# Kernel tuning notes

Hardware: AMD Instinct MI355X
Metric: run time of the kernel (lower is better)

The kernel has to match this reference:

```python
import jax, jax.numpy as jnp
import numpy as np

N_DOMAINS = 8
LN_EPS = 1e-5


def setup_inputs() -> dict:
    key = jax.random.key(0)
    ks = jax.random.split(key, 4)
    N, D_IN, D_HID, D_OUT = 32768, 256, 1024, 256
    x = jax.random.normal(ks[0], (N, D_IN), dtype=jnp.float32)
    domain_types = jax.random.randint(ks[1], (N,), 0, N_DOMAINS, dtype=jnp.int32)
    # Per-domain MLP parameters (8 independent experts)
    W1 = jax.random.normal(ks[2], (N_DOMAINS, D_IN, D_HID), dtype=jnp.float32) * (1.0 / np.sqrt(D_IN))
    b1 = jnp.zeros((N_DOMAINS, D_HID), dtype=jnp.float32)
    gamma = jnp.ones((N_DOMAINS, D_HID), dtype=jnp.float32)
    beta = jnp.zeros((N_DOMAINS, D_HID), dtype=jnp.float32)
    W2 = jax.random.normal(ks[3], (N_DOMAINS, D_HID, D_OUT), dtype=jnp.float32) * (1.0 / np.sqrt(D_HID))
    b2 = jnp.zeros((N_DOMAINS, D_OUT), dtype=jnp.float32)
    return {"x": x, "domain_types": domain_types, "W1": W1, "b1": b1,
            "gamma": gamma, "beta": beta, "W2": W2, "b2": b2}


def _expert_mlp(x, W1d, b1d, gd, bd, W2d, b2d):
    # Linear -> LayerNorm -> ReLU -> (Dropout: identity at eval) -> Linear
    h = x @ W1d + b1d                       # [N, hid]
    mu = jnp.mean(h, axis=-1, keepdims=True)
    var = jnp.mean(jnp.square(h - mu), axis=-1, keepdims=True)
    h = (h - mu) * jax.lax.rsqrt(var + LN_EPS) * gd + bd
    h = jax.nn.relu(h)
    return h @ W2d + b2d                    # [N, out]


def reference(x, domain_types, W1, b1, gamma, beta, W2, b2):
    # output dim == x.shape[-1] (as in the torch code: zeros(batch, x.shape[-1]))
    out = jnp.zeros((x.shape[0], x.shape[-1]), dtype=x.dtype)
    for d in range(N_DOMAINS):  # small fixed expert loop (static MoE dispatch)
        y = _expert_mlp(x, W1[d], b1[d], gamma[d], beta[d], W2[d], b2[d])
        mask = (domain_types == d)[:, None]
        out = jnp.where(mask, y, out)
    return out
```

## Files before the change

### kernel.cpp

```cpp
#include <hip/hip_runtime.h>
#include <hip/hip_bf16.h>


#define ND 8
#define NROWS 32768
#define DIN 256
#define DHID 1024
#define DOUT 256
#define MPAD 33792
#define NTILES 264

typedef short short8 __attribute__((ext_vector_type(8)));
typedef unsigned short ushort8v __attribute__((ext_vector_type(8)));
typedef float floatx4 __attribute__((ext_vector_type(4)));

__device__ __forceinline__ unsigned short f2bf(float f) {
    unsigned u = __builtin_bit_cast(unsigned, f);
    unsigned r = u + 0x7fff + ((u >> 16) & 1);
    return (unsigned short)(r >> 16);
}
__device__ __forceinline__ float bf2f(unsigned short h) {
    unsigned u = ((unsigned)h) << 16;
    return __builtin_bit_cast(float, u);
}

#define GLDS16(gp, lp) __builtin_amdgcn_global_load_lds( \
    (const __attribute__((address_space(1))) void*)(gp), \
    (__attribute__((address_space(3))) void*)(lp), 16, 0, 0)

__global__ void transpose_both(const float* __restrict__ W1,
                               const float* __restrict__ W2,
                               unsigned short* __restrict__ W1T,
                               unsigned short* __restrict__ W2T,
                               int* __restrict__ cnt) {
    __shared__ float t[32][33];
    const int z = blockIdx.z;
    const bool isW1 = z < ND;
    const int d = isW1 ? z : z - ND;
    const int R = isW1 ? DIN : DHID;
    const int C = isW1 ? DHID : DOUT;
    const int r0 = (isW1 ? blockIdx.x : blockIdx.y) * 32;
    const int c0 = (isW1 ? blockIdx.y : blockIdx.x) * 32;
    const int tx = threadIdx.x & 31, ty = threadIdx.x >> 5;
    if (z == 0 && blockIdx.x == 0 && blockIdx.y == 0 && threadIdx.x < 16)
        cnt[threadIdx.x] = 0;
    const float* src = (isW1 ? W1 : W2) + (size_t)d * R * C;
    unsigned short* dst = (isW1 ? W1T : W2T) + (size_t)d * R * C;
#pragma unroll
    for (int i = 0; i < 32; i += 8)
        t[ty + i][tx] = src[(size_t)(r0 + ty + i) * C + c0 + tx];
    __syncthreads();
#pragma unroll
    for (int i = 0; i < 32; i += 8)
        dst[(size_t)(c0 + ty + i) * R + r0 + tx] = f2bf(t[tx][ty + i]);
}

__global__ void histo(const int* __restrict__ dt, int* __restrict__ counts) {
    __shared__ int lc[ND];
    if (threadIdx.x < ND) lc[threadIdx.x] = 0;
    __syncthreads();
    int i = blockIdx.x * 256 + threadIdx.x;
    atomicAdd(&lc[dt[i]], 1);
    __syncthreads();
    if (threadIdx.x < ND) atomicAdd(&counts[threadIdx.x], lc[threadIdx.x]);
}

__global__ void make_meta(const int* __restrict__ counts, int* __restrict__ cursors,
                          int2* __restrict__ meta, int* __restrict__ perm) {
    __shared__ int ps[ND], pe[ND];
    if (threadIdx.x == 0) {
        int off = 0, t = 0;
        for (int d = 0; d < ND; d++) {
            cursors[d] = off;
            int nt = (counts[d] + 127) >> 7;
            for (int i = 0; i < nt; i++) meta[t++] = make_int2(d, off + (i << 7));
            ps[d] = off + counts[d];
            pe[d] = off + (nt << 7);
            off += nt << 7;
        }
        for (; t < NTILES; t++) meta[t] = make_int2(-1, 0);
    }
    __syncthreads();
#pragma unroll
    for (int d = 0; d < ND; d++)
        for (int p = ps[d] + threadIdx.x; p < pe[d]; p += 256) perm[p] = -1;
}

__global__ __launch_bounds__(256)
void assign_pos(const int* __restrict__ dt, int* __restrict__ cursors,
                int* __restrict__ perm, int* __restrict__ pos) {
    __shared__ int lcnt[ND];
    __shared__ int lbase[ND];
    const int tid = threadIdx.x;
    if (tid < ND) lcnt[tid] = 0;
    __syncthreads();
    const int r = blockIdx.x * 256 + tid;
    const int d = dt[r];
    const int myrank = atomicAdd(&lcnt[d], 1);
    __syncthreads();
    if (tid < ND && lcnt[tid] > 0)
        lbase[tid] = atomicAdd(&cursors[tid], lcnt[tid]);
    __syncthreads();
    const int p = lbase[d] + myrank;
    pos[r] = p;
    perm[p] = r;
}

__global__ __launch_bounds__(256)
void copy_rows(const float* __restrict__ x, const int* __restrict__ pos,
               unsigned short* __restrict__ xs) {
    const int tid = threadIdx.x;
    const int lane = tid & 63;
    const int r = blockIdx.x * 4 + (tid >> 6);
    const int p = pos[r];
    float4 v = ((const float4*)(x + (size_t)r * DIN))[lane];
    ushort4 o;
    o.x = f2bf(v.x); o.y = f2bf(v.y); o.z = f2bf(v.z); o.w = f2bf(v.w);
    ((ushort4*)(xs + (size_t)p * DIN))[lane] = o;
}

__global__ __launch_bounds__(256, 2)
void gemm_a(const unsigned short* __restrict__ A,
            const unsigned short* __restrict__ Bt,
            const float* __restrict__ bias,
            const int2* __restrict__ meta,
            unsigned short* __restrict__ H,
            float2* __restrict__ stats) {
    const int2 md = meta[blockIdx.x];
    const int dom = md.x;
    if (dom < 0) return;
    const int m0 = md.y;
    const int n0 = blockIdx.y * 256;

    __shared__ unsigned short As[128 * 32];
    __shared__ unsigned short Bs[256 * 32];

    const int tid = threadIdx.x;
    const int lane = tid & 63;
    const int w = tid >> 6;
    const int wr = w >> 1, wc = w & 1;
    const int c16 = lane & 15, quad = lane >> 4;

    const unsigned short* Abase = A + (size_t)m0 * DIN;
    const unsigned short* Bbase = Bt + (size_t)dom * DHID * DIN + (size_t)n0 * DIN;

    floatx4 acc[4][8];
#pragma unroll
    for (int i = 0; i < 4; i++)
#pragma unroll
        for (int j = 0; j < 8; j++) acc[i][j] = 0.f;

    for (int k0 = 0; k0 < DIN; k0 += 32) {
#pragma unroll
        for (int it = 0; it < 2; ++it) {
            const int c = w * 128 + it * 64 + lane;
            const int m = c >> 2, kc = c & 3;
            GLDS16(Abase + (size_t)m * DIN + k0 + kc * 8, &As[(w * 128 + it * 64) * 8]);
        }
#pragma unroll
        for (int it = 0; it < 4; ++it) {
            const int c = w * 256 + it * 64 + lane;
            const int n = c >> 2, kc = c & 3;
            GLDS16(Bbase + (size_t)n * DIN + k0 + kc * 8, &Bs[(w * 256 + it * 64) * 8]);
        }
        __syncthreads();

        short8 a[4], b[8];
        const int kk = quad * 8;
#pragma unroll
        for (int i = 0; i < 4; i++)
            a[i] = *(const short8*)&As[(wr * 64 + i * 16 + c16) * 32 + kk];
#pragma unroll
        for (int j = 0; j < 8; j++)
            b[j] = *(const short8*)&Bs[(wc * 128 + j * 16 + c16) * 32 + kk];
#pragma unroll
        for (int i = 0; i < 4; i++)
#pragma unroll
            for (int j = 0; j < 8; j++)
                acc[i][j] = __builtin_amdgcn_mfma_f32_16x16x32_bf16(a[i], b[j], acc[i][j], 0, 0, 0);
        __syncthreads();
    }

    float bv[8];
#pragma unroll
    for (int j = 0; j < 8; j++)
        bv[j] = bias[dom * DHID + n0 + wc * 128 + j * 16 + c16];

    float2* st = stats + (size_t)(blockIdx.y * 2 + wc) * MPAD;
#pragma unroll
    for (int i = 0; i < 4; i++) {
        const int rowbase = m0 + wr * 64 + i * 16 + quad * 4;
#pragma unroll
        for (int r = 0; r < 4; r++) {
            float s = 0.f, q = 0.f;
            unsigned short* hrow = H + (size_t)(rowbase + r) * DHID + n0 + wc * 128;
#pragma unroll
            for (int j = 0; j < 8; j++) {
                const float v = acc[i][j][r] + bv[j];
                hrow[j * 16 + c16] = f2bf(v);
                s += v; q += v * v;
            }
#pragma unroll
            for (int o = 1; o < 16; o <<= 1) {
                s += __shfl_xor(s, o, 64);
                q += __shfl_xor(q, o, 64);
            }
            if (c16 == 0) st[rowbase + r] = make_float2(s, q);
        }
    }
}

__global__ __launch_bounds__(256, 1)
void gemm_b_ln(const unsigned short* __restrict__ H,
               const unsigned short* __restrict__ Bt,
               const float* __restrict__ bias,
               const float* __restrict__ gamma,
               const float* __restrict__ beta,
               const float2* __restrict__ stats,
               const int2* __restrict__ meta,
               const int* __restrict__ perm,
               float* __restrict__ out) {
    const int2 md = meta[blockIdx.x];
    const int dom = md.x;
    if (dom < 0) return;
    const int m0 = md.y;

    __shared__ unsigned short As[128 * 32];
    __shared__ unsigned short Bs[256 * 32];
    __shared__ unsigned short gsh[DHID];
    __shared__ unsigned short bsh[DHID];
    __shared__ float mu_s[128], rs_s[128];

    const int tid = threadIdx.x;
    const int lane = tid & 63;
    const int w = tid >> 6;
    const int wr = w >> 1, wc = w & 1;
    const int c16 = lane & 15, quad = lane >> 4;

    if (tid < 128) {
        float s = 0.f, q = 0.f;
#pragma unroll
        for (int cb = 0; cb < 8; cb++) {
            const float2 p = stats[(size_t)cb * MPAD + m0 + tid];
            s += p.x; q += p.y;
        }
        const float inv = 1.0f / (float)DHID;
        const float mu = s * inv;
        const float var = fmaxf(q * inv - mu * mu, 0.f);
        mu_s[tid] = mu;
        rs_s[tid] = rsqrtf(var + 1e-5f);
    }
    {
        const int base = tid * 4;
        const float4 g4 = *(const float4*)(gamma + dom * DHID + base);
        const float4 b4 = *(const float4*)(beta + dom * DHID + base);
        gsh[base + 0] = f2bf(g4.x); gsh[base + 1] = f2bf(g4.y);
        gsh[base + 2] = f2bf(g4.z); gsh[base + 3] = f2bf(g4.w);
        bsh[base + 0] = f2bf(b4.x); bsh[base + 1] = f2bf(b4.y);
        bsh[base + 2] = f2bf(b4.z); bsh[base + 3] = f2bf(b4.w);
    }
    __syncthreads();

    const unsigned short* Hbase = H + (size_t)m0 * DHID;
    const unsigned short* Bbase = Bt + (size_t)dom * DOUT * DHID;

    floatx4 acc[4][8];
#pragma unroll
    for (int i = 0; i < 4; i++)
#pragma unroll
        for (int j = 0; j < 8; j++) acc[i][j] = 0.f;

    const int c0i = tid, c1i = 256 + tid;
    const int row0 = c0i >> 2, kg0 = c0i & 3;
    const int row1 = c1i >> 2, kg1 = c1i & 3;
    ushort8v hv0 = *(const ushort8v*)(Hbase + (size_t)row0 * DHID + kg0 * 8);
    ushort8v hv1 = *(const ushort8v*)(Hbase + (size_t)row1 * DHID + kg1 * 8);

    for (int k0 = 0; k0 < DHID; k0 += 32) {
        {
            const float mu0 = mu_s[row0], rs0 = rs_s[row0];
            const float mu1 = mu_s[row1], rs1 = rs_s[row1];
            const ushort8v g0 = *(const ushort8v*)&gsh[k0 + kg0 * 8];
            const ushort8v b0 = *(const ushort8v*)&bsh[k0 + kg0 * 8];
            const ushort8v g1 = *(const ushort8v*)&gsh[k0 + kg1 * 8];
            const ushort8v b1v = *(const ushort8v*)&bsh[k0 + kg1 * 8];
            ushort8v o0, o1;
#pragma unroll
            for (int e = 0; e < 8; e++) {
                const float t0 = (bf2f(hv0[e]) - mu0) * rs0;
                o0[e] = f2bf(fmaxf(t0 * bf2f(g0[e]) + bf2f(b0[e]), 0.f));
                const float t1 = (bf2f(hv1[e]) - mu1) * rs1;
                o1[e] = f2bf(fmaxf(t1 * bf2f(g1[e]) + bf2f(b1v[e]), 0.f));
            }
            *(ushort8v*)&As[row0 * 32 + kg0 * 8] = o0;
            *(ushort8v*)&As[row1 * 32 + kg1 * 8] = o1;
        }
#pragma unroll
        for (int it = 0; it < 4; ++it) {
            const int c = w * 256 + it * 64 + lane;
            const int n = c >> 2, kc = c & 3;
            GLDS16(Bbase + (size_t)n * DHID + k0 + kc * 8, &Bs[(w * 256 + it * 64) * 8]);
        }
        if (k0 + 32 < DHID) {
            hv0 = *(const ushort8v*)(Hbase + (size_t)row0 * DHID + k0 + 32 + kg0 * 8);
            hv1 = *(const ushort8v*)(Hbase + (size_t)row1 * DHID + k0 + 32 + kg1 * 8);
        }
        __syncthreads();

        short8 a[4], b[8];
        const int kk = quad * 8;
#pragma unroll
        for (int i = 0; i < 4; i++)
            a[i] = *(const short8*)&As[(wr * 64 + i * 16 + c16) * 32 + kk];
#pragma unroll
        for (int j = 0; j < 8; j++)
            b[j] = *(const short8*)&Bs[(wc * 128 + j * 16 + c16) * 32 + kk];
#pragma unroll
        for (int i = 0; i < 4; i++)
#pragma unroll
            for (int j = 0; j < 8; j++)
                acc[i][j] = __builtin_amdgcn_mfma_f32_16x16x32_bf16(a[i], b[j], acc[i][j], 0, 0, 0);
        __syncthreads();
    }

    float bv[8];
#pragma unroll
    for (int j = 0; j < 8; j++)
        bv[j] = bias[dom * DOUT + wc * 128 + j * 16 + c16];
#pragma unroll
    for (int i = 0; i < 4; i++) {
        const int rowbase = m0 + wr * 64 + i * 16 + quad * 4;
#pragma unroll
        for (int r = 0; r < 4; r++) {
            const int orig = perm[rowbase + r];
            if (orig < 0) continue;
#pragma unroll
            for (int j = 0; j < 8; j++) {
                const int col = wc * 128 + j * 16 + c16;
                out[(size_t)orig * DOUT + col] = acc[i][j][r] + bv[j];
            }
        }
    }
}

extern "C" void kernel_launch(void* const* d_in, const int* in_sizes, int n_in,
                              void* d_out, int out_size, void* d_ws, size_t ws_size,
                              hipStream_t stream) {
    const float* x = (const float*)d_in[0];
    const int* dt = (const int*)d_in[1];
    const float* W1 = (const float*)d_in[2];
    const float* b1 = (const float*)d_in[3];
    const float* gamma = (const float*)d_in[4];
    const float* beta = (const float*)d_in[5];
    const float* W2 = (const float*)d_in[6];
    const float* b2 = (const float*)d_in[7];
    float* out = (float*)d_out;

    char* ws = (char*)d_ws;
    size_t off = 0;
    auto take = [&](size_t nbytes) -> char* {
        char* p = ws + off;
        off = (off + nbytes + 255) & ~(size_t)255;
        return p;
    };
    unsigned short* W1T = (unsigned short*)take((size_t)ND * DHID * DIN * 2);
    unsigned short* W2T = (unsigned short*)take((size_t)ND * DOUT * DHID * 2);
    unsigned short* XS  = (unsigned short*)take((size_t)MPAD * DIN * 2);
    unsigned short* H   = (unsigned short*)take((size_t)MPAD * DHID * 2);
    float2* STATS = (float2*)take((size_t)8 * MPAD * 8);
    int* PERM   = (int*)take(MPAD * 4);
    int* POS    = (int*)take(NROWS * 4);
    int* CNT    = (int*)take(64);
    int2* META  = (int2*)take(NTILES * 8);
    (void)ws_size; (void)n_in; (void)in_sizes; (void)out_size;

    int* COUNTS = CNT;
    int* CURSORS = CNT + 8;

    transpose_both<<<dim3(8, 32, 16), 256, 0, stream>>>(W1, W2, W1T, W2T, CNT);
    histo<<<NROWS / 256, 256, 0, stream>>>(dt, COUNTS);
    make_meta<<<1, 256, 0, stream>>>(COUNTS, CURSORS, META, PERM);
    assign_pos<<<NROWS / 256, 256, 0, stream>>>(dt, CURSORS, PERM, POS);
    copy_rows<<<NROWS / 4, 256, 0, stream>>>(x, POS, XS);
    gemm_a<<<dim3(NTILES, 4), 256, 0, stream>>>(XS, W1T, b1, META, H, STATS);
    gemm_b_ln<<<NTILES, 256, 0, stream>>>(
        H, W2T, b2, gamma, beta, STATS, META, PERM, out);
}
```

Measured before the change: 246.9 us.

## Split LayerNorm out of second GEMM, fuse histogram and row-copy kernels

Merges the histogram into the weight-transpose launch as an extra z-slice, and merges position assignment with the bf16 row copy so the pos buffer and one launch go away. The LayerNorm+ReLU that ran inside the second GEMM's k-loop becomes a separate in-place pass over H. The second GEMM becomes a plain 128x128 tile GEMM with async global-to-LDS loads for both operands, giving twice as many blocks and higher occupancy. In exchange, H now takes an extra read and write through global memory, and the row copy uses only 128 blocks.

```diff
diff --git a/kernel.cpp b/kernel.cpp
--- a/kernel.cpp
+++ b/kernel.cpp
@@ -28,13 +28,25 @@
     (const __attribute__((address_space(1))) void*)(gp), \
     (__attribute__((address_space(3))) void*)(lp), 16, 0, 0)
 
-__global__ void transpose_both(const float* __restrict__ W1,
-                               const float* __restrict__ W2,
-                               unsigned short* __restrict__ W1T,
-                               unsigned short* __restrict__ W2T,
-                               int* __restrict__ cnt) {
+__global__ void transpose_histo(const float* __restrict__ W1,
+                                const float* __restrict__ W2,
+                                unsigned short* __restrict__ W1T,
+                                unsigned short* __restrict__ W2T,
+                                const int* __restrict__ dt,
+                                int* __restrict__ counts) {
+    const int z = blockIdx.z;
+    if (z == 16) {
+        const int bid = blockIdx.y * 8 + blockIdx.x;
+        if (bid >= NROWS / 256) return;
+        __shared__ int lc[ND];
+        if (threadIdx.x < ND) lc[threadIdx.x] = 0;
+        __syncthreads();
+        atomicAdd(&lc[dt[bid * 256 + threadIdx.x]], 1);
+        __syncthreads();
+        if (threadIdx.x < ND) atomicAdd(&counts[threadIdx.x], lc[threadIdx.x]);
+        return;
+    }
     __shared__ float t[32][33];
-    const int z = blockIdx.z;
     const bool isW1 = z < ND;
     const int d = isW1 ? z : z - ND;
     const int R = isW1 ? DIN : DHID;
@@ -42,8 +54,6 @@
     const int r0 = (isW1 ? blockIdx.x : blockIdx.y) * 32;
     const int c0 = (isW1 ? blockIdx.y : blockIdx.x) * 32;
     const int tx = threadIdx.x & 31, ty = threadIdx.x >> 5;
-    if (z == 0 && blockIdx.x == 0 && blockIdx.y == 0 && threadIdx.x < 16)
-        cnt[threadIdx.x] = 0;
     const float* src = (isW1 ? W1 : W2) + (size_t)d * R * C;
     unsigned short* dst = (isW1 ? W1T : W2T) + (size_t)d * R * C;
 #pragma unroll
@@ -53,16 +63,6 @@
 #pragma unroll
     for (int i = 0; i < 32; i += 8)
         dst[(size_t)(c0 + ty + i) * R + r0 + tx] = f2bf(t[tx][ty + i]);
-}
-
-__global__ void histo(const int* __restrict__ dt, int* __restrict__ counts) {
-    __shared__ int lc[ND];
-    if (threadIdx.x < ND) lc[threadIdx.x] = 0;
-    __syncthreads();
-    int i = blockIdx.x * 256 + threadIdx.x;
-    atomicAdd(&lc[dt[i]], 1);
-    __syncthreads();
-    if (threadIdx.x < ND) atomicAdd(&counts[threadIdx.x], lc[threadIdx.x]);
 }
 
 __global__ void make_meta(const int* __restrict__ counts, int* __restrict__ cursors,
@@ -87,10 +87,11 @@
 }
 
 __global__ __launch_bounds__(256)
-void assign_pos(const int* __restrict__ dt, int* __restrict__ cursors,
-                int* __restrict__ perm, int* __restrict__ pos) {
-    __shared__ int lcnt[ND];
-    __shared__ int lbase[ND];
+void assign_copy(const float* __restrict__ x, const int* __restrict__ dt,
+                 int* __restrict__ cursors, int* __restrict__ perm,
+                 unsigned short* __restrict__ xs) {
+    __shared__ int lcnt[ND], lbase[ND];
+    __shared__ int spos[256];
     const int tid = threadIdx.x;
     if (tid < ND) lcnt[tid] = 0;
     __syncthreads();
@@ -102,21 +103,20 @@
         lbase[tid] = atomicAdd(&cursors[tid], lcnt[tid]);
     __syncthreads();
     const int p = lbase[d] + myrank;
-    pos[r] = p;
+    spos[tid] = p;
     perm[p] = r;
-}
-
-__global__ __launch_bounds__(256)
-void copy_rows(const float* __restrict__ x, const int* __restrict__ pos,
-               unsigned short* __restrict__ xs) {
-    const int tid = threadIdx.x;
+    __syncthreads();
     const int lane = tid & 63;
-    const int r = blockIdx.x * 4 + (tid >> 6);
-    const int p = pos[r];
-    float4 v = ((const float4*)(x + (size_t)r * DIN))[lane];
-    ushort4 o;
-    o.x = f2bf(v.x); o.y = f2bf(v.y); o.z = f2bf(v.z); o.w = f2bf(v.w);
-    ((ushort4*)(xs + (size_t)p * DIN))[lane] = o;
+    const int sub = tid >> 6;
+    for (int it = 0; it < 64; ++it) {
+        const int lr = it * 4 + sub;
+        const int gr = blockIdx.x * 256 + lr;
+        const int pp = spos[lr];
+        float4 v = ((const float4*)(x + (size_t)gr * DIN))[lane];
+        ushort4 o;
+        o.x = f2bf(v.x); o.y = f2bf(v.y); o.z = f2bf(v.z); o.w = f2bf(v.w);
+        ((ushort4*)(xs + (size_t)pp * DIN))[lane] = o;
+    }
 }
 
 __global__ __launch_bounds__(256, 2)
@@ -210,26 +210,69 @@
     }
 }
 
-__global__ __launch_bounds__(256, 1)
-void gemm_b_ln(const unsigned short* __restrict__ H,
-               const unsigned short* __restrict__ Bt,
-               const float* __restrict__ bias,
-               const float* __restrict__ gamma,
-               const float* __restrict__ beta,
-               const float2* __restrict__ stats,
-               const int2* __restrict__ meta,
-               const int* __restrict__ perm,
-               float* __restrict__ out) {
+__global__ __launch_bounds__(256)
+void ln_relu(unsigned short* __restrict__ H,
+             const float* __restrict__ gamma, const float* __restrict__ beta,
+             const float2* __restrict__ stats, const int2* __restrict__ meta) {
+    const int2 md = meta[blockIdx.x >> 2];
+    const int dom = md.x;
+    if (dom < 0) return;
+    const int m0 = md.y + (blockIdx.x & 3) * 32;
+
+    __shared__ float mu_s[32], rs_s[32];
+    const int tid = threadIdx.x;
+    if (tid < 32) {
+        float s = 0.f, q = 0.f;
+#pragma unroll
+        for (int cb = 0; cb < 8; cb++) {
+            const float2 p = stats[(size_t)cb * MPAD + m0 + tid];
+            s += p.x; q += p.y;
+        }
+        const float inv = 1.0f / (float)DHID;
+        const float mu = s * inv;
+        const float var = fmaxf(q * inv - mu * mu, 0.f);
+        mu_s[tid] = mu;
+        rs_s[tid] = rsqrtf(var + 1e-5f);
+    }
+    const int cc = (tid & 127) * 8;
+    const float4 g0 = *(const float4*)(gamma + dom * DHID + cc);
+    const float4 g1 = *(const float4*)(gamma + dom * DHID + cc + 4);
+    const float4 b0 = *(const float4*)(beta + dom * DHID + cc);
+    const float4 b1 = *(const float4*)(beta + dom * DHID + cc + 4);
+    const float gg[8] = {g0.x, g0.y, g0.z, g0.w, g1.x, g1.y, g1.z, g1.w};
+    const float bb[8] = {b0.x, b0.y, b0.z, b0.w, b1.x, b1.y, b1.z, b1.w};
+    __syncthreads();
+
+    const int half = tid >> 7;
+#pragma unroll 4
+    for (int it = 0; it < 16; ++it) {
+        const int lr = it * 2 + half;
+        unsigned short* hp = H + (size_t)(m0 + lr) * DHID + cc;
+        const ushort8v hv = *(const ushort8v*)hp;
+        const float mu = mu_s[lr], rs = rs_s[lr];
+        ushort8v o;
+#pragma unroll
+        for (int e = 0; e < 8; e++)
+            o[e] = f2bf(fmaxf((bf2f(hv[e]) - mu) * rs * gg[e] + bb[e], 0.f));
+        *(ushort8v*)hp = o;
+    }
+}
+
+__global__ __launch_bounds__(256, 2)
+void gemm_bt(const unsigned short* __restrict__ A,
+             const unsigned short* __restrict__ Bt,
+             const float* __restrict__ bias,
+             const int2* __restrict__ meta,
+             const int* __restrict__ perm,
+             float* __restrict__ out) {
     const int2 md = meta[blockIdx.x];
     const int dom = md.x;
     if (dom < 0) return;
     const int m0 = md.y;
+    const int n0 = blockIdx.y * 128;
 
     __shared__ unsigned short As[128 * 32];
-    __shared__ unsigned short Bs[256 * 32];
-    __shared__ unsigned short gsh[DHID];
-    __shared__ unsigned short bsh[DHID];
-    __shared__ float mu_s[128], rs_s[128];
+    __shared__ unsigned short Bs[128 * 32];
 
     const int tid = threadIdx.x;
     const int lane = tid & 63;
@@ -237,96 +280,40 @@
     const int wr = w >> 1, wc = w & 1;
     const int c16 = lane & 15, quad = lane >> 4;
 
-    if (tid < 128) {
-        float s = 0.f, q = 0.f;
-#pragma unroll
-        for (int cb = 0; cb < 8; cb++) {
-            const float2 p = stats[(size_t)cb * MPAD + m0 + tid];
-            s += p.x; q += p.y;
-        }
-        const float inv = 1.0f / (float)DHID;
-        const float mu = s * inv;
-        const float var = fmaxf(q * inv - mu * mu, 0.f);
-        mu_s[tid] = mu;
-        rs_s[tid] = rsqrtf(var + 1e-5f);
-    }
-    {
-        const int base = tid * 4;
-        const float4 g4 = *(const float4*)(gamma + dom * DHID + base);
-        const float4 b4 = *(const float4*)(beta + dom * DHID + base);
-        gsh[base + 0] = f2bf(g4.x); gsh[base + 1] = f2bf(g4.y);
-        gsh[base + 2] = f2bf(g4.z); gsh[base + 3] = f2bf(g4.w);
-        bsh[base + 0] = f2bf(b4.x); bsh[base + 1] = f2bf(b4.y);
-        bsh[base + 2] = f2bf(b4.z); bsh[base + 3] = f2bf(b4.w);
-    }
-    __syncthreads();
-
-    const unsigned short* Hbase = H + (size_t)m0 * DHID;
-    const unsigned short* Bbase = Bt + (size_t)dom * DOUT * DHID;
-
-    floatx4 acc[4][8];
+    const unsigned short* Abase = A + (size_t)m0 * DHID;
+    const unsigned short* Bbase = Bt + (size_t)dom * DOUT * DHID + (size_t)n0 * DHID;
+
+    floatx4 acc[4][4];
 #pragma unroll
     for (int i = 0; i < 4; i++)
 #pragma unroll
-        for (int j = 0; j < 8; j++) acc[i][j] = 0.f;
-
-    const int c0i = tid, c1i = 256 + tid;
-    const int row0 = c0i >> 2, kg0 = c0i & 3;
-    const int row1 = c1i >> 2, kg1 = c1i & 3;
-    ushort8v hv0 = *(const ushort8v*)(Hbase + (size_t)row0 * DHID + kg0 * 8);
-    ushort8v hv1 = *(const ushort8v*)(Hbase + (size_t)row1 * DHID + kg1 * 8);
+        for (int j = 0; j < 4; j++) acc[i][j] = 0.f;
 
     for (int k0 = 0; k0 < DHID; k0 += 32) {
-        {
-            const float mu0 = mu_s[row0], rs0 = rs_s[row0];
-            const float mu1 = mu_s[row1], rs1 = rs_s[row1];
-            const ushort8v g0 = *(const ushort8v*)&gsh[k0 + kg0 * 8];
-            const ushort8v b0 = *(const ushort8v*)&bsh[k0 + kg0 * 8];
-            const ushort8v g1 = *(const ushort8v*)&gsh[k0 + kg1 * 8];
-            const ushort8v b1v = *(const ushort8v*)&bsh[k0 + kg1 * 8];
-            ushort8v o0, o1;
-#pragma unroll
-            for (int e = 0; e < 8; e++) {
-                const float t0 = (bf2f(hv0[e]) - mu0) * rs0;
-                o0[e] = f2bf(fmaxf(t0 * bf2f(g0[e]) + bf2f(b0[e]), 0.f));
-                const float t1 = (bf2f(hv1[e]) - mu1) * rs1;
-                o1[e] = f2bf(fmaxf(t1 * bf2f(g1[e]) + bf2f(b1v[e]), 0.f));
-            }
-            *(ushort8v*)&As[row0 * 32 + kg0 * 8] = o0;
-            *(ushort8v*)&As[row1 * 32 + kg1 * 8] = o1;
-        }
-#pragma unroll
-        for (int it = 0; it < 4; ++it) {
-            const int c = w * 256 + it * 64 + lane;
-            const int n = c >> 2, kc = c & 3;
-            GLDS16(Bbase + (size_t)n * DHID + k0 + kc * 8, &Bs[(w * 256 + it * 64) * 8]);
-        }
-        if (k0 + 32 < DHID) {
-            hv0 = *(const ushort8v*)(Hbase + (size_t)row0 * DHID + k0 + 32 + kg0 * 8);
-            hv1 = *(const ushort8v*)(Hbase + (size_t)row1 * DHID + k0 + 32 + kg1 * 8);
-        }
-        __syncthreads();
-
-        short8 a[4], b[8];
+#pragma unroll
+        for (int it = 0; it < 2; ++it) {
+            const int c = w * 128 + it * 64 + lane;
+            const int m = c >> 2, kc = c & 3;
+            GLDS16(Abase + (size_t)m * DHID + k0 + kc * 8, &As[(w * 128 + it * 64) * 8]);
+            GLDS16(Bbase + (size_t)m * DHID + k0 + kc * 8, &Bs[(w * 128 + it * 64) * 8]);
+        }
+        __syncthreads();
+
+        short8 a[4], b[4];
         const int kk = quad * 8;
 #pragma unroll
+        for (int i = 0; i < 4; i++) {
+            a[i] = *(const short8*)&As[(wr * 64 + i * 16 + c16) * 32 + kk];
+            b[i] = *(const short8*)&Bs[(wc * 64 + i * 16 + c16) * 32 + kk];
+        }
+#pragma unroll
         for (int i = 0; i < 4; i++)
-            a[i] = *(const short8*)&As[(wr * 64 + i * 16 + c16) * 32 + kk];
-#pragma unroll
-        for (int j = 0; j < 8; j++)
-            b[j] = *(const short8*)&Bs[(wc * 128 + j * 16 + c16) * 32 + kk];
-#pragma unroll
-        for (int i = 0; i < 4; i++)
-#pragma unroll
-            for (int j = 0; j < 8; j++)
+#pragma unroll
+            for (int j = 0; j < 4; j++)
                 acc[i][j] = __builtin_amdgcn_mfma_f32_16x16x32_bf16(a[i], b[j], acc[i][j], 0, 0, 0);
         __syncthreads();
     }
 
-    float bv[8];
-#pragma unroll
-    for (int j = 0; j < 8; j++)
-        bv[j] = bias[dom * DOUT + wc * 128 + j * 16 + c16];
 #pragma unroll
     for (int i = 0; i < 4; i++) {
         const int rowbase = m0 + wr * 64 + i * 16 + quad * 4;
@@ -335,9 +322,9 @@
             const int orig = perm[rowbase + r];
             if (orig < 0) continue;
 #pragma unroll
-            for (int j = 0; j < 8; j++) {
-                const int col = wc * 128 + j * 16 + c16;
-                out[(size_t)orig * DOUT + col] = acc[i][j][r] + bv[j];
+            for (int j = 0; j < 4; j++) {
+                const int col = n0 + wc * 64 + j * 16 + c16;
+                out[(size_t)orig * DOUT + col] = acc[i][j][r] + bias[dom * DOUT + col];
             }
         }
     }
@@ -369,7 +356,6 @@
     unsigned short* H   = (unsigned short*)take((size_t)MPAD * DHID * 2);
     float2* STATS = (float2*)take((size_t)8 * MPAD * 8);
     int* PERM   = (int*)take(MPAD * 4);
-    int* POS    = (int*)take(NROWS * 4);
     int* CNT    = (int*)take(64);
     int2* META  = (int2*)take(NTILES * 8);
     (void)ws_size; (void)n_in; (void)in_sizes; (void)out_size;
@@ -377,12 +363,11 @@
     int* COUNTS = CNT;
     int* CURSORS = CNT + 8;
 
-    transpose_both<<<dim3(8, 32, 16), 256, 0, stream>>>(W1, W2, W1T, W2T, CNT);
-    histo<<<NROWS / 256, 256, 0, stream>>>(dt, COUNTS);
+    hipMemsetAsync(CNT, 0, 64, stream);
+    transpose_histo<<<dim3(8, 32, 17), 256, 0, stream>>>(W1, W2, W1T, W2T, dt, COUNTS);
     make_meta<<<1, 256, 0, stream>>>(COUNTS, CURSORS, META, PERM);
-    assign_pos<<<NROWS / 256, 256, 0, stream>>>(dt, CURSORS, PERM, POS);
-    copy_rows<<<NROWS / 4, 256, 0, stream>>>(x, POS, XS);
+    assign_copy<<<NROWS / 256, 256, 0, stream>>>(x, dt, CURSORS, PERM, XS);
     gemm_a<<<dim3(NTILES, 4), 256, 0, stream>>>(XS, W1T, b1, META, H, STATS);
-    gemm_b_ln<<<NTILES, 256, 0, stream>>>(
-        H, W2T, b2, gamma, beta, STATS, META, PERM, out);
-}
+    ln_relu<<<NTILES * 4, 256, 0, stream>>>(H, gamma, beta, STATS, META);
+    gemm_bt<<<dim3(NTILES, 2), 256, 0, stream>>>(H, W2T, b2, META, PERM, out);
+}
```

New measurement: 228.8 us. -7.3%, faster.
